# Performance work log

Measured on AMD Instinct MI355X. Metric: run time of the kernel, lower is better.

## Reference

```python
import jax, jax.numpy as jnp
import numpy as np

KEEP_P = 0.75  # 1 - dropout_p, dropout_p = 0.25

def setup_inputs() -> dict:
    key = jax.random.key(0)
    k1, k2, k3, k4 = jax.random.split(key, 4)
    B, Sq, Skv, D, Dv = 8, 2048, 2048, 128, 128
    x1 = jax.random.normal(k1, (B, Sq, D), dtype=jnp.float32)
    x2 = jax.random.normal(k2, (B, Skv, D), dtype=jnp.float32)
    x3 = jax.random.normal(k3, (B, Skv, Dv), dtype=jnp.float32)
    # torch Dropout(p): mask = bernoulli(keep_p) / keep_p
    keep = jax.random.bernoulli(k4, KEEP_P, (B, Sq, Skv))
    dropout_mask = keep.astype(jnp.float32) / KEEP_P
    return {"x1": x1, "x2": x2, "x3": x3, "dropout_mask": dropout_mask}

def reference(x1, x2, x3, dropout_mask):
    # scores: [B, Sq, Skv] = x1 @ x2^T (no scale: scale_factor is None)
    scores = jnp.einsum("bqd,bkd->bqk", x1, x2)
    probs = jax.nn.softmax(scores, axis=-1)
    probs = probs * dropout_mask  # dropout with fixed mask
    out = jnp.einsum("bqk,bkv->bqv", probs, x3)  # [B, Sq, Dv]
    return out
```

## Files before the change

kernel.cpp:

```cpp
#include <hip/hip_runtime.h>
#include <stdint.h>

#define SQ 2048
#define SKV 2048
#define DD 128
#define NB 8
#define M0 40.0f
#define LOG2E 1.44269504088896340736f

typedef float    f4v __attribute__((ext_vector_type(4)));
typedef __bf16   bf8 __attribute__((ext_vector_type(8)));
typedef _Float16 h8  __attribute__((ext_vector_type(8)));

__device__ __forceinline__ void async16(const void* g, void* l) {
    __builtin_amdgcn_global_load_lds(
        (const __attribute__((address_space(1))) void*)g,
        (__attribute__((address_space(3))) void*)l, 16, 0, 0);
}

__global__ void cast_f16_swz(const float* __restrict__ src,
                             _Float16* __restrict__ dst) {
    int tid = blockIdx.x * 256 + threadIdx.x;
    int d8 = tid & 15;
    int kv = (tid >> 4) & (SKV - 1);
    int b  = tid >> 15;
    const float* p = src + ((size_t)b * SKV + kv) * DD + d8 * 8;
    f4v a0 = *(const f4v*)p;
    f4v a1 = *(const f4v*)(p + 4);
    h8 h;
#pragma unroll
    for (int c = 0; c < 4; c++) {
        h[c]     = (_Float16)a0[c];
        h[c + 4] = (_Float16)a1[c];
    }
    int s = d8 >> 2, g = d8 & 3, kb32 = kv >> 5, row = kv & 31;
    *(h8*)(dst + (size_t)(b * 64 + kb32) * 4096 + (size_t)((s * 32 + row) * 4 + g) * 8) = h;
}

__global__ void transpose_v_swz(const float* __restrict__ v, __bf16* __restrict__ vtf) {
    __shared__ __bf16 tile[32][33];
    int kb32 = blockIdx.x, dv0 = blockIdx.y * 32, b = blockIdx.z;
    int tx = threadIdx.x, ty = threadIdx.y;
    const float* src = v + ((size_t)b * SKV + kb32 * 32 + ty) * DD + dv0 + tx;
#pragma unroll
    for (int i = 0; i < 32; i += 8)
        tile[ty + i][tx] = (__bf16)src[(size_t)i * DD];
    __syncthreads();
    int pcol = (tx < 16) ? ((tx >> 2) << 3) + (tx & 3)
                         : (((tx - 16) >> 2) << 3) + 4 + (tx & 3);
    __bf16* dst = vtf + (size_t)(b * 64 + kb32) * 4096 + pcol;
#pragma unroll
    for (int i = 0; i < 32; i += 8)
        dst[(size_t)(dv0 + ty + i) * 32] = tile[tx][ty + i];
}

__global__ __launch_bounds__(256, 2) void attn_kernel(
    const float* __restrict__ Qf, const _Float16* __restrict__ Kh,
    const __bf16* __restrict__ Vt, const float* __restrict__ mask,
    float* __restrict__ O_part, float* __restrict__ l_part,
    int nsp, int kv_len) {
    __shared__ __align__(16) char smem[2][16384];
    const int lin = blockIdx.x;
    const int per_xcd = (NB * nsp) >> 3;
    const int xcd = lin & 7;
    const int idx = lin >> 3;
    const int slice = xcd * per_xcd + (idx >> 4);
    const int qblk = idx & 15;
    const int b = slice / nsp, sid = slice % nsp;
    const int tid = threadIdx.x;
    const int w = tid >> 6, lane = tid & 63;
    const int g = lane >> 4, n = lane & 15;
    const int qb = qblk * 128 + w * 32;
    const int kv0 = sid * kv_len;
    const int kb32_0 = kv0 >> 5;
    const int niter = kv_len >> 5;

    const _Float16* Kt0 = Kh + (size_t)(b * 64 + kb32_0) * 4096;
    const __bf16*   Vt0 = Vt + (size_t)(b * 64 + kb32_0) * 4096;
    auto stage = [&](int buf, int it) {
#pragma unroll
        for (int jj = 0; jj < 4; jj++) {
            int j = w * 4 + jj;
            if (j < 8)
                async16(Kt0 + (size_t)it * 4096 + j * 512 + lane * 8,
                        (void*)&smem[buf][j * 1024]);
            else
                async16(Vt0 + (size_t)it * 4096 + (j - 8) * 512 + lane * 8,
                        (void*)&smem[buf][8192 + (j - 8) * 1024]);
        }
    };
    stage(0, 0);

    h8 qf[2][4];
#pragma unroll
    for (int u = 0; u < 2; u++) {
        const float* Qrow = Qf + ((size_t)b * SQ + qb + u * 16 + n) * DD + g * 8;
#pragma unroll
        for (int s = 0; s < 4; s++) {
            f4v v0 = *(const f4v*)(Qrow + s * 32);
            f4v v1 = *(const f4v*)(Qrow + s * 32 + 4);
#pragma unroll
            for (int c = 0; c < 4; c++) {
                qf[u][s][c]     = (_Float16)v0[c];
                qf[u][s][c + 4] = (_Float16)v1[c];
            }
        }
    }

    const float* mrow0 = mask + ((size_t)b * SQ + qb + n) * SKV + kv0;
    const float* mrow1 = mrow0 + (size_t)16 * SKV;
    f4v c00 = *(const f4v*)(mrow0 + g * 4);
    f4v c01 = *(const f4v*)(mrow0 + 16 + g * 4);
    f4v c10 = *(const f4v*)(mrow1 + g * 4);
    f4v c11 = *(const f4v*)(mrow1 + 16 + g * 4);

    const f4v zero = {0.f, 0.f, 0.f, 0.f};
    f4v o0[8], o1[8];
#pragma unroll
    for (int t = 0; t < 8; t++) { o0[t] = zero; o1[t] = zero; }
    float l0 = 0.f, l1 = 0.f;

    for (int it = 0; it < niter; it++) {
        __syncthreads();

        if (it + 1 < niter) stage((it + 1) & 1, it + 1);
        const int itn = (it + 1 < niter) ? it + 1 : it;
        f4v n00 = *(const f4v*)(mrow0 + itn * 32 + g * 4);
        f4v n01 = *(const f4v*)(mrow0 + itn * 32 + 16 + g * 4);
        f4v n10 = *(const f4v*)(mrow1 + itn * 32 + g * 4);
        f4v n11 = *(const f4v*)(mrow1 + itn * 32 + 16 + g * 4);

        const _Float16* Lk = (const _Float16*)smem[it & 1];
        const __bf16*   Lv = (const __bf16*)(smem[it & 1] + 8192);

        f4v s00 = zero, s01 = zero, s10 = zero, s11 = zero;
#pragma unroll
        for (int s = 0; s < 4; s++) {
            h8 a0 = *(const h8*)(Lk + (size_t)((s * 32 + n) * 4 + g) * 8);
            h8 a1 = *(const h8*)(Lk + (size_t)((s * 32 + n + 16) * 4 + g) * 8);
            s00 = __builtin_amdgcn_mfma_f32_16x16x32_f16(a0, qf[0][s], s00, 0, 0, 0);
            s01 = __builtin_amdgcn_mfma_f32_16x16x32_f16(a1, qf[0][s], s01, 0, 0, 0);
            s10 = __builtin_amdgcn_mfma_f32_16x16x32_f16(a0, qf[1][s], s10, 0, 0, 0);
            s11 = __builtin_amdgcn_mfma_f32_16x16x32_f16(a1, qf[1][s], s11, 0, 0, 0);
        }

        bf8 pf0, pf1;
#pragma unroll
        for (int r = 0; r < 4; r++) {
            float e00 = exp2f(s00[r] * LOG2E - M0 * LOG2E);
            float e01 = exp2f(s01[r] * LOG2E - M0 * LOG2E);
            float e10 = exp2f(s10[r] * LOG2E - M0 * LOG2E);
            float e11 = exp2f(s11[r] * LOG2E - M0 * LOG2E);
            l0 += e00 + e01;
            l1 += e10 + e11;
            pf0[r]     = (__bf16)(e00 * c00[r]);
            pf0[r + 4] = (__bf16)(e01 * c01[r]);
            pf1[r]     = (__bf16)(e10 * c10[r]);
            pf1[r + 4] = (__bf16)(e11 * c11[r]);
        }

#pragma unroll
        for (int t = 0; t < 8; t++) {
            bf8 vf = *(const bf8*)(Lv + (size_t)((t * 16 + n) * 4 + g) * 8);
            o0[t] = __builtin_amdgcn_mfma_f32_16x16x32_bf16(pf0, vf, o0[t], 0, 0, 0);
            o1[t] = __builtin_amdgcn_mfma_f32_16x16x32_bf16(pf1, vf, o1[t], 0, 0, 0);
        }
        c00 = n00; c01 = n01; c10 = n10; c11 = n11;
    }

    l0 += __shfl_xor(l0, 16); l0 += __shfl_xor(l0, 32);
    l1 += __shfl_xor(l1, 16); l1 += __shfl_xor(l1, 32);
    const int qt = qblk * 8 + w * 2;
    const int tile0 = (b * 128 + qt) * nsp + sid;
    const int tile1 = (b * 128 + qt + 1) * nsp + sid;
    float* op0 = O_part + (size_t)tile0 * 2048;
    float* op1 = O_part + (size_t)tile1 * 2048;
#pragma unroll
    for (int t = 0; t < 8; t++)
#pragma unroll
        for (int r = 0; r < 4; r++) {
            op0[(g * 4 + r) * 128 + t * 16 + n] = o0[t][r];
            op1[(g * 4 + r) * 128 + t * 16 + n] = o1[t][r];
        }
    if (g == 0) {
        l_part[(size_t)tile0 * 16 + n] = l0;
        l_part[(size_t)tile1 * 16 + n] = l1;
    }
}

__global__ __launch_bounds__(256) void combine_kernel(
    const float* __restrict__ O_part, const float* __restrict__ l_part,
    float* __restrict__ out, int nsp) {
    const int qt = blockIdx.x;
    const int b  = blockIdx.y;
    const int tbase = (b * 128 + qt) * nsp;
    const int q  = threadIdx.x >> 4;
    const int d8 = threadIdx.x & 15;
    f4v a0 = {0.f, 0.f, 0.f, 0.f}, a1 = {0.f, 0.f, 0.f, 0.f};
    float L = 0.f;
    for (int s = 0; s < nsp; s++) {
        const float* op = O_part + (size_t)(tbase + s) * 2048 + q * 128 + d8 * 8;
        a0 += *(const f4v*)op;
        a1 += *(const f4v*)(op + 4);
        L  += l_part[(size_t)(tbase + s) * 16 + q];
    }
    float scale = 1.0f / L;
    float* o = out + ((size_t)b * SQ + qt * 16 + q) * DD + d8 * 8;
    *(f4v*)o       = a0 * scale;
    *(f4v*)(o + 4) = a1 * scale;
}

extern "C" void kernel_launch(void* const* d_in, const int* in_sizes, int n_in,
                              void* d_out, int out_size, void* d_ws, size_t ws_size,
                              hipStream_t stream) {
    const float* x1   = (const float*)d_in[0];
    const float* x2   = (const float*)d_in[1];
    const float* x3   = (const float*)d_in[2];
    const float* mask = (const float*)d_in[3];
    float* out = (float*)d_out;

    const size_t kelems = (size_t)NB * SKV * DD;
    _Float16* Kh  = (_Float16*)d_ws;
    __bf16*   VTf = (__bf16*)(Kh + kelems);
    float*    O_part = (float*)(VTf + kelems);

    size_t base = 2 * kelems * 2;
    size_t per  = (size_t)NB * 128 * (2048 + 16) * sizeof(float);
    int nsp = 4;
    while (nsp > 1 && base + (size_t)nsp * per > ws_size) nsp >>= 1;
    float* l_part = O_part + (size_t)NB * 128 * nsp * 2048;

    hipLaunchKernelGGL(cast_f16_swz, dim3(NB * SKV * 16 / 256), dim3(256), 0, stream,
                       x2, Kh);
    hipLaunchKernelGGL(transpose_v_swz, dim3(SKV / 32, DD / 32, NB), dim3(32, 8), 0,
                       stream, x3, VTf);
    hipLaunchKernelGGL(attn_kernel, dim3(16 * NB * nsp), dim3(256), 0, stream,
                       x1, Kh, VTf, mask, O_part, l_part, nsp, SKV / nsp);
    hipLaunchKernelGGL(combine_kernel, dim3(128, NB), dim3(256), 0, stream,
                       O_part, l_part, out, nsp);
}
```

Before: 233.6 us.

## Triple-buffer K/V staging with explicit vmcnt waits and fuse preprocess kernels

Moves the attention loop from double to triple buffering in LDS. It prefetches K/V tiles and mask values two iterations ahead, using a partial s_waitcnt vmcnt(8) plus a raw barrier in place of __syncthreads, so more global loads stay in flight. It also merges the K cast and V transpose kernels into one launch and folds the softmax offset constant. LDS use rises to 48KB per block, which may limit occupancy, and the manual vmcnt count depends on the exact number of loads issued.

Result: no change. 233.8 us (+0.1%).

```diff
diff --git a/kernel.cpp b/kernel.cpp
--- a/kernel.cpp
+++ b/kernel.cpp
@@ -5,8 +5,8 @@
 #define SKV 2048
 #define DD 128
 #define NB 8
-#define M0 40.0f
 #define LOG2E 1.44269504088896340736f
+#define M0L 57.70780163555852f
 
 typedef float    f4v __attribute__((ext_vector_type(4)));
 typedef __bf16   bf8 __attribute__((ext_vector_type(8)));
@@ -18,40 +18,42 @@
         (__attribute__((address_space(3))) void*)l, 16, 0, 0);
 }
 
-__global__ void cast_f16_swz(const float* __restrict__ src,
-                             _Float16* __restrict__ dst) {
-    int tid = blockIdx.x * 256 + threadIdx.x;
-    int d8 = tid & 15;
-    int kv = (tid >> 4) & (SKV - 1);
-    int b  = tid >> 15;
-    const float* p = src + ((size_t)b * SKV + kv) * DD + d8 * 8;
-    f4v a0 = *(const f4v*)p;
-    f4v a1 = *(const f4v*)(p + 4);
-    h8 h;
-#pragma unroll
-    for (int c = 0; c < 4; c++) {
-        h[c]     = (_Float16)a0[c];
-        h[c + 4] = (_Float16)a1[c];
-    }
-    int s = d8 >> 2, g = d8 & 3, kb32 = kv >> 5, row = kv & 31;
-    *(h8*)(dst + (size_t)(b * 64 + kb32) * 4096 + (size_t)((s * 32 + row) * 4 + g) * 8) = h;
-}
-
-__global__ void transpose_v_swz(const float* __restrict__ v, __bf16* __restrict__ vtf) {
+__global__ void preprocess(const float* __restrict__ x2, _Float16* __restrict__ Kh,
+                           const float* __restrict__ x3, __bf16* __restrict__ VTf) {
     __shared__ __bf16 tile[32][33];
-    int kb32 = blockIdx.x, dv0 = blockIdx.y * 32, b = blockIdx.z;
-    int tx = threadIdx.x, ty = threadIdx.y;
-    const float* src = v + ((size_t)b * SKV + kb32 * 32 + ty) * DD + dv0 + tx;
-#pragma unroll
-    for (int i = 0; i < 32; i += 8)
-        tile[ty + i][tx] = (__bf16)src[(size_t)i * DD];
-    __syncthreads();
-    int pcol = (tx < 16) ? ((tx >> 2) << 3) + (tx & 3)
-                         : (((tx - 16) >> 2) << 3) + 4 + (tx & 3);
-    __bf16* dst = vtf + (size_t)(b * 64 + kb32) * 4096 + pcol;
-#pragma unroll
-    for (int i = 0; i < 32; i += 8)
-        dst[(size_t)(dv0 + ty + i) * 32] = tile[tx][ty + i];
+    const int bid = blockIdx.x;
+    if (bid < 1024) {
+        int tid = bid * 256 + threadIdx.x;
+        int d8 = tid & 15;
+        int kv = (tid >> 4) & (SKV - 1);
+        int b  = tid >> 15;
+        const float* p = x2 + ((size_t)b * SKV + kv) * DD + d8 * 8;
+        f4v a0 = *(const f4v*)p;
+        f4v a1 = *(const f4v*)(p + 4);
+        h8 h;
+#pragma unroll
+        for (int c = 0; c < 4; c++) {
+            h[c]     = (_Float16)a0[c];
+            h[c + 4] = (_Float16)a1[c];
+        }
+        int s = d8 >> 2, g = d8 & 3, kb32 = kv >> 5, row = kv & 31;
+        *(h8*)(Kh + (size_t)(b * 64 + kb32) * 4096 + (size_t)((s * 32 + row) * 4 + g) * 8) = h;
+    } else {
+        int t = bid - 1024;
+        int kb32 = t & 63, dv0 = ((t >> 6) & 3) * 32, b = t >> 8;
+        int tx = threadIdx.x & 31, ty = threadIdx.x >> 5;
+        const float* src = x3 + ((size_t)b * SKV + kb32 * 32 + ty) * DD + dv0 + tx;
+#pragma unroll
+        for (int i = 0; i < 32; i += 8)
+            tile[ty + i][tx] = (__bf16)src[(size_t)i * DD];
+        __syncthreads();
+        int pcol = (tx < 16) ? ((tx >> 2) << 3) + (tx & 3)
+                             : (((tx - 16) >> 2) << 3) + 4 + (tx & 3);
+        __bf16* dst = VTf + (size_t)(b * 64 + kb32) * 4096 + pcol;
+#pragma unroll
+        for (int i = 0; i < 32; i += 8)
+            dst[(size_t)(dv0 + ty + i) * 32] = tile[tx][ty + i];
+    }
 }
 
 __global__ __launch_bounds__(256, 2) void attn_kernel(
@@ -59,7 +61,7 @@
     const __bf16* __restrict__ Vt, const float* __restrict__ mask,
     float* __restrict__ O_part, float* __restrict__ l_part,
     int nsp, int kv_len) {
-    __shared__ __align__(16) char smem[2][16384];
+    __shared__ __align__(16) char smem[3][16384];
     const int lin = blockIdx.x;
     const int per_xcd = (NB * nsp) >> 3;
     const int xcd = lin & 7;
@@ -77,19 +79,18 @@
 
     const _Float16* Kt0 = Kh + (size_t)(b * 64 + kb32_0) * 4096;
     const __bf16*   Vt0 = Vt + (size_t)(b * 64 + kb32_0) * 4096;
-    auto stage = [&](int buf, int it) {
+    auto stageTo = [&](char* buf, int it) {
 #pragma unroll
         for (int jj = 0; jj < 4; jj++) {
             int j = w * 4 + jj;
             if (j < 8)
                 async16(Kt0 + (size_t)it * 4096 + j * 512 + lane * 8,
-                        (void*)&smem[buf][j * 1024]);
+                        (void*)(buf + j * 1024));
             else
                 async16(Vt0 + (size_t)it * 4096 + (j - 8) * 512 + lane * 8,
-                        (void*)&smem[buf][8192 + (j - 8) * 1024]);
+                        (void*)(buf + 8192 + (j - 8) * 1024));
         }
     };
-    stage(0, 0);
 
     h8 qf[2][4];
 #pragma unroll
@@ -109,10 +110,6 @@
 
     const float* mrow0 = mask + ((size_t)b * SQ + qb + n) * SKV + kv0;
     const float* mrow1 = mrow0 + (size_t)16 * SKV;
-    f4v c00 = *(const f4v*)(mrow0 + g * 4);
-    f4v c01 = *(const f4v*)(mrow0 + 16 + g * 4);
-    f4v c10 = *(const f4v*)(mrow1 + g * 4);
-    f4v c11 = *(const f4v*)(mrow1 + 16 + g * 4);
 
     const f4v zero = {0.f, 0.f, 0.f, 0.f};
     f4v o0[8], o1[8];
@@ -120,18 +117,41 @@
     for (int t = 0; t < 8; t++) { o0[t] = zero; o1[t] = zero; }
     float l0 = 0.f, l1 = 0.f;
 
-    for (int it = 0; it < niter; it++) {
-        __syncthreads();
-
-        if (it + 1 < niter) stage((it + 1) & 1, it + 1);
-        const int itn = (it + 1 < niter) ? it + 1 : it;
-        f4v n00 = *(const f4v*)(mrow0 + itn * 32 + g * 4);
-        f4v n01 = *(const f4v*)(mrow0 + itn * 32 + 16 + g * 4);
-        f4v n10 = *(const f4v*)(mrow1 + itn * 32 + g * 4);
-        f4v n11 = *(const f4v*)(mrow1 + itn * 32 + 16 + g * 4);
-
-        const _Float16* Lk = (const _Float16*)smem[it & 1];
-        const __bf16*   Lv = (const __bf16*)(smem[it & 1] + 8192);
+    char* s0p = &smem[0][0];
+    char* s1p = &smem[1][0];
+    char* s2p = &smem[2][0];
+
+    stageTo(s0p, 0);
+    asm volatile("" ::: "memory");
+    f4v mA00 = *(const f4v*)(mrow0 + g * 4);
+    f4v mA01 = *(const f4v*)(mrow0 + 16 + g * 4);
+    f4v mA10 = *(const f4v*)(mrow1 + g * 4);
+    f4v mA11 = *(const f4v*)(mrow1 + 16 + g * 4);
+    asm volatile("" ::: "memory");
+    const int it1 = (1 < niter) ? 1 : 0;
+    stageTo(s1p, it1);
+    asm volatile("" ::: "memory");
+    f4v mB00 = *(const f4v*)(mrow0 + it1 * 32 + g * 4);
+    f4v mB01 = *(const f4v*)(mrow0 + it1 * 32 + 16 + g * 4);
+    f4v mB10 = *(const f4v*)(mrow1 + it1 * 32 + g * 4);
+    f4v mB11 = *(const f4v*)(mrow1 + it1 * 32 + 16 + g * 4);
+    f4v mC00 = zero, mC01 = zero, mC10 = zero, mC11 = zero;
+
+    auto body = [&](int it, const char* bufR, char* bufW,
+                    const f4v& u00, const f4v& u01, const f4v& u10, const f4v& u11,
+                    f4v& t00, f4v& t01, f4v& t10, f4v& t11) {
+        asm volatile("s_waitcnt vmcnt(8)" ::: "memory");
+        __builtin_amdgcn_s_barrier();
+        asm volatile("" ::: "memory");
+        const int itp = (it + 2 < niter) ? it + 2 : niter - 1;
+        stageTo(bufW, itp);
+        t00 = *(const f4v*)(mrow0 + itp * 32 + g * 4);
+        t01 = *(const f4v*)(mrow0 + itp * 32 + 16 + g * 4);
+        t10 = *(const f4v*)(mrow1 + itp * 32 + g * 4);
+        t11 = *(const f4v*)(mrow1 + itp * 32 + 16 + g * 4);
+
+        const _Float16* Lk = (const _Float16*)bufR;
+        const __bf16*   Lv = (const __bf16*)(bufR + 8192);
 
         f4v s00 = zero, s01 = zero, s10 = zero, s11 = zero;
 #pragma unroll
@@ -147,16 +167,16 @@
         bf8 pf0, pf1;
 #pragma unroll
         for (int r = 0; r < 4; r++) {
-            float e00 = exp2f(s00[r] * LOG2E - M0 * LOG2E);
-            float e01 = exp2f(s01[r] * LOG2E - M0 * LOG2E);
-            float e10 = exp2f(s10[r] * LOG2E - M0 * LOG2E);
-            float e11 = exp2f(s11[r] * LOG2E - M0 * LOG2E);
+            float e00 = exp2f(s00[r] * LOG2E - M0L);
+            float e01 = exp2f(s01[r] * LOG2E - M0L);
+            float e10 = exp2f(s10[r] * LOG2E - M0L);
+            float e11 = exp2f(s11[r] * LOG2E - M0L);
             l0 += e00 + e01;
             l1 += e10 + e11;
-            pf0[r]     = (__bf16)(e00 * c00[r]);
-            pf0[r + 4] = (__bf16)(e01 * c01[r]);
-            pf1[r]     = (__bf16)(e10 * c10[r]);
-            pf1[r + 4] = (__bf16)(e11 * c11[r]);
+            pf0[r]     = (__bf16)(e00 * u00[r]);
+            pf0[r + 4] = (__bf16)(e01 * u01[r]);
+            pf1[r]     = (__bf16)(e10 * u10[r]);
+            pf1[r + 4] = (__bf16)(e11 * u11[r]);
         }
 
 #pragma unroll
@@ -165,7 +185,14 @@
             o0[t] = __builtin_amdgcn_mfma_f32_16x16x32_bf16(pf0, vf, o0[t], 0, 0, 0);
             o1[t] = __builtin_amdgcn_mfma_f32_16x16x32_bf16(pf1, vf, o1[t], 0, 0, 0);
         }
-        c00 = n00; c01 = n01; c10 = n10; c11 = n11;
+    };
+
+    for (int it = 0; it < niter; it += 3) {
+        body(it,     s0p, s2p, mA00, mA01, mA10, mA11, mC00, mC01, mC10, mC11);
+        if (it + 1 < niter)
+            body(it + 1, s1p, s0p, mB00, mB01, mB10, mB11, mA00, mA01, mA10, mA11);
+        if (it + 2 < niter)
+            body(it + 2, s2p, s1p, mC00, mC01, mC10, mC11, mB00, mB01, mB10, mB11);
     }
 
     l0 += __shfl_xor(l0, 16); l0 += __shfl_xor(l0, 32);
@@ -230,10 +257,8 @@
     while (nsp > 1 && base + (size_t)nsp * per > ws_size) nsp >>= 1;
     float* l_part = O_part + (size_t)NB * 128 * nsp * 2048;
 
-    hipLaunchKernelGGL(cast_f16_swz, dim3(NB * SKV * 16 / 256), dim3(256), 0, stream,
-                       x2, Kh);
-    hipLaunchKernelGGL(transpose_v_swz, dim3(SKV / 32, DD / 32, NB), dim3(32, 8), 0,
-                       stream, x3, VTf);
+    hipLaunchKernelGGL(preprocess, dim3(3072), dim3(256), 0, stream,
+                       x2, Kh, x3, VTf);
     hipLaunchKernelGGL(attn_kernel, dim3(16 * NB * nsp), dim3(256), 0, stream,
                        x1, Kh, VTf, mask, O_part, l_part, nsp, SKV / nsp);
     hipLaunchKernelGGL(combine_kernel, dim3(128, NB), dim3(256), 0, stream,
```
